# Kernel optimization log

Hardware: AMD Instinct MI355X
Metric: run time of the kernel (lower is better)

Reference implementation:

```python
import jax, jax.numpy as jnp
import numpy as np

EMBED_DIM = 256
H = 80
W = 80
N_HEADS = 8
N_POINTS = 4
B = 8


def sine_pe(C, h, w):
    # LoFTR-style PositionEncodingSine, returns [1, C, h, w]
    y_pos = jnp.cumsum(jnp.ones((h, w), jnp.float32), axis=0)[None]
    x_pos = jnp.cumsum(jnp.ones((h, w), jnp.float32), axis=1)[None]
    div = jnp.exp(jnp.arange(0, C // 2, 2, dtype=jnp.float32) * (-np.log(10000.0) / (C // 2)))[:, None, None]
    pe = jnp.zeros((C, h, w), jnp.float32)
    pe = pe.at[0::4].set(jnp.sin(x_pos * div))
    pe = pe.at[1::4].set(jnp.cos(x_pos * div))
    pe = pe.at[2::4].set(jnp.sin(y_pos * div))
    pe = pe.at[3::4].set(jnp.cos(y_pos * div))
    return pe[None]


def make_reference_points(h, w):
    # Faithful to the original (W-major flatten, (col, row) stacking)
    gr = np.linspace(0, 1, w)
    gc = np.linspace(0, 1, h)
    R, Cg = np.meshgrid(gr, gc, indexing='ij')  # (w, h)
    ref = np.stack((Cg, R), -1).reshape(-1, 2)  # [w*h, 2]
    return jnp.asarray(ref, jnp.float32)


def setup_inputs():
    key = jax.random.key(0)
    ks = jax.random.split(key, 8)
    C = EMBED_DIM
    s = 1.0 / np.sqrt(C)
    return {
        'query': jax.random.normal(ks[0], (B, C, H, W), jnp.float32),
        'value': jax.random.normal(ks[1], (B, C, H, W), jnp.float32),
        'W_value': jax.random.normal(ks[2], (C, C), jnp.float32) * s,
        'b_value': jnp.zeros((C,), jnp.float32),
        'W_off': jax.random.normal(ks[3], (C, N_HEADS * N_POINTS * 2), jnp.float32) * 0.01,
        'b_off': jax.random.normal(ks[4], (N_HEADS * N_POINTS * 2,), jnp.float32) * 0.5,
        'W_attn': jax.random.normal(ks[5], (C, N_HEADS * N_POINTS), jnp.float32) * s,
        'b_attn': jnp.zeros((N_HEADS * N_POINTS,), jnp.float32),
        'W_out': jax.random.normal(ks[6], (C, C), jnp.float32) * s,
        'b_out': jnp.zeros((C,), jnp.float32),
    }


def _deform_attn_core(q, v, ref, W_off, b_off, W_attn, b_attn):
    # q: [B, Nq, C] queries; v: [B, H*W, C] projected values; ref: [Nq, 2]
    Bq, Nq, C = q.shape
    hd = C // N_HEADS
    off = (q @ W_off + b_off).reshape(Bq, Nq, N_HEADS, N_POINTS, 2)
    aw = jax.nn.softmax((q @ W_attn + b_attn).reshape(Bq, Nq, N_HEADS, N_POINTS), axis=-1)
    norm = jnp.array([W, H], jnp.float32)  # offset normalizer (W, H), num_levels=1
    loc = ref[None, :, None, None, :] + off / norm  # [B, Nq, Hn, P, 2], normalized (x, y)
    loc = loc.transpose(0, 2, 1, 3, 4)  # [B, Hn, Nq, P, 2]
    # grid_sample(align_corners=False, padding_mode='zeros'): pixel = loc*size - 0.5
    x = loc[..., 0] * W - 0.5
    y = loc[..., 1] * H - 0.5
    x0f = jnp.floor(x); y0f = jnp.floor(y)
    wx = x - x0f; wy = y - y0f
    x0 = x0f.astype(jnp.int32); y0 = y0f.astype(jnp.int32)
    vh = v.reshape(Bq, H * W, N_HEADS, hd).transpose(0, 2, 1, 3)  # [B, Hn, HW, hd]

    def gather(ix, iy):
        valid = (ix >= 0) & (ix < W) & (iy >= 0) & (iy < H)
        idx = jnp.clip(iy, 0, H - 1) * W + jnp.clip(ix, 0, W - 1)  # [B, Hn, Nq, P]
        g = jnp.take_along_axis(vh, idx.reshape(Bq, N_HEADS, -1, 1), axis=2)
        return g.reshape(Bq, N_HEADS, Nq, N_POINTS, hd) * valid[..., None].astype(v.dtype)

    samp = (gather(x0, y0) * ((1 - wx) * (1 - wy))[..., None]
            + gather(x0 + 1, y0) * (wx * (1 - wy))[..., None]
            + gather(x0, y0 + 1) * ((1 - wx) * wy)[..., None]
            + gather(x0 + 1, y0 + 1) * (wx * wy)[..., None])  # [B, Hn, Nq, P, hd]
    out = jnp.einsum('bhqpd,bhqp->bqhd', samp, aw.transpose(0, 2, 1, 3))
    return out.reshape(Bq, Nq, C)


def reference(query, value, W_value, b_value, W_off, b_off, W_attn, b_attn, W_out, b_out):
    pe = sine_pe(EMBED_DIM, H, W)
    q = query + pe
    qf = q.reshape(B, EMBED_DIM, H * W).transpose(0, 2, 1)      # [B, Nq, C]
    vf = value.reshape(B, EMBED_DIM, H * W).transpose(0, 2, 1)  # [B, Nv, C]
    vproj = vf @ W_value + b_value
    ref = make_reference_points(H, W)
    attn = _deform_attn_core(qf, vproj, ref, W_off, b_off, W_attn, b_attn)
    attn = attn @ W_out + b_out
    attn = attn + qf  # mmcv MSDeformAttn residual (dropout identity at eval)
    out_img = attn.transpose(0, 2, 1).reshape(B, EMBED_DIM, H, W)
    # nn.Upsample(size=(H, W), bilinear) on an (H, W) map is identity (need_downsample=False)
    return (out_img + value, out_img)
```

## Files before the change

kernel.cpp:

```cpp
#include <hip/hip_runtime.h>
#include <hip/hip_bf16.h>
#include <stdint.h>

#define HH 80
#define WW 80
#define NQ 6400
#define CD 256
#define BB 8
#define OUT_HALF 13107200
#define PE_NEG 0.0719557841560639f

typedef __attribute__((ext_vector_type(4))) float f32x4;
typedef __bf16 bf16_t;
typedef __attribute__((ext_vector_type(8))) __bf16 bf16x8;

using gp1_t = const __attribute__((address_space(1))) void*;
using lp3_t = __attribute__((address_space(3))) void*;

__device__ __forceinline__ void gload_lds16(const void* g, void* l) {
    __builtin_amdgcn_global_load_lds((gp1_t)g, (lp3_t)l, 16, 0, 0);
}

__global__ __launch_bounds__(256) void wprep_kernel(const float* __restrict__ Wv,
                                                    const float* __restrict__ Woff,
                                                    const float* __restrict__ Wattn,
                                                    const float* __restrict__ Wout,
                                                    bf16_t* __restrict__ WvT,
                                                    bf16_t* __restrict__ WoaT,
                                                    bf16_t* __restrict__ WoT) {
    int idx = blockIdx.x * 256 + threadIdx.x;
    if (idx < 65536) {
        int cp = idx >> 8, c = idx & 255;
        WvT[idx] = (bf16_t)Wv[c * 256 + cp];
        WoT[idx] = (bf16_t)Wout[c * 256 + cp];
    }
    if (idx < 96 * 256) {
        int j = idx >> 8, c = idx & 255;
        WoaT[idx] = (bf16_t)(j < 64 ? Woff[c * 64 + j] : Wattn[c * 32 + (j - 64)]);
    }
}

__global__ __launch_bounds__(256, 3) void gemm_vproj(const float* __restrict__ V,
                                                     const bf16_t* __restrict__ Y,
                                                     const float* __restrict__ bias,
                                                     bf16_t* __restrict__ D) {
    __shared__ __align__(16) bf16_t lx[128 * 72];
    __shared__ __align__(16) bf16_t ly[128 * 64];
    int b = blockIdx.x & 7;
    int nloc = (blockIdx.x >> 3) * 128;
    int m0 = b * NQ + nloc;
    int c0 = blockIdx.y * 128;
    const float* src = V + (size_t)b * CD * NQ + nloc;
    int tid = threadIdx.x, wv = tid >> 6, ln = tid & 63;
    f32x4 acc[4][4] = {};
    int wr = (wv >> 1) * 64, wc = (wv & 1) * 64;
    int nl = tid & 31;
    for (int kt = 0; kt < 4; ++kt) {
#pragma unroll
        for (int q8 = 0; q8 < 4; ++q8) {
            int q = wv * 4 + q8;
            int row = q * 8 + (ln >> 3);
            int jj = (ln & 7) ^ (row & 7);
            gload_lds16((const char*)Y + ((size_t)(c0 + row)) * 512 + (size_t)kt * 128 + jj * 16,
                        (char*)ly + q * 1024);
        }
#pragma unroll
        for (int i = 0; i < 4; ++i) {
            int kp = (tid >> 5) + i * 8;
            int k = kp * 2;
            const float* s0 = src + (size_t)(kt * 64 + k) * NQ;
#pragma unroll
            for (int l = 0; l < 4; ++l) {
                int n = nl + 32 * l;
                float v0 = s0[n];
                float v1 = s0[NQ + n];
                union { bf16_t h[2]; uint32_t u; } pk;
                pk.h[0] = (bf16_t)v0; pk.h[1] = (bf16_t)v1;
                *(uint32_t*)((char*)lx + n * 144 + k * 2) = pk.u;
            }
        }
        __syncthreads();
#pragma unroll
        for (int ks = 0; ks < 2; ++ks) {
            bf16x8 xa[4], yb[4];
#pragma unroll
            for (int i = 0; i < 4; i++) {
                int m = wr + i * 16 + (ln & 15);
                xa[i] = *(const bf16x8*)((const char*)lx + m * 144 + ks * 64 + (ln >> 4) * 16);
                int n = wc + i * 16 + (ln & 15);
                int cn = (ks * 4 + (ln >> 4)) ^ (n & 7);
                yb[i] = *(const bf16x8*)((const char*)ly + n * 128 + cn * 16);
            }
#pragma unroll
            for (int i = 0; i < 4; i++)
#pragma unroll
                for (int j = 0; j < 4; j++)
                    acc[i][j] = __builtin_amdgcn_mfma_f32_16x16x32_bf16(xa[i], yb[j], acc[i][j], 0, 0, 0);
        }
        __syncthreads();
    }
#pragma unroll
    for (int i = 0; i < 4; i++)
#pragma unroll
        for (int j = 0; j < 4; j++) {
            int col = c0 + wc + j * 16 + (ln & 15);
            float bv = bias[col];
#pragma unroll
            for (int rg = 0; rg < 4; rg++) {
                int row = m0 + wr + i * 16 + (ln >> 4) * 4 + rg;
                D[(size_t)row * 256 + col] = (bf16_t)(acc[i][j][rg] + bv);
            }
        }
}

__global__ __launch_bounds__(256, 3) void oa_sample_out(
        const float* __restrict__ Q,
        const bf16_t* __restrict__ Woa,
        const float* __restrict__ boff,
        const float* __restrict__ battn,
        const bf16_t* __restrict__ vp,
        const bf16_t* __restrict__ WoT,
        const float* __restrict__ bout,
        const float* __restrict__ value,
        float* __restrict__ out) {
    __shared__ __align__(16) char smem[54272];
    char* sampL = smem;
    bf16_t* lx = (bf16_t*)(smem + 32768);
    bf16_t* ly = (bf16_t*)(smem + 41984);
    bf16_t* oaT = (bf16_t*)(smem + 32768);
    bf16_t* wx = (bf16_t*)(smem + 32768);
    float* tile = (float*)(smem + 32768);

    int bid = blockIdx.x;
    int b = bid & 7;
    int nloc = (bid >> 3) * 64;
    int tid = threadIdx.x, wv = tid >> 6, ln = tid & 63;
    const float* src = Q + (size_t)b * CD * NQ + nloc;
    int nl = tid & 31;

    f32x4 accA[6] = {};
    for (int kt = 0; kt < 4; ++kt) {
#pragma unroll
        for (int q3 = 0; q3 < 3; ++q3) {
            int q = wv * 3 + q3;
            int row = q * 8 + (ln >> 3);
            int jj = (ln & 7) ^ (row & 7);
            gload_lds16((const char*)Woa + ((size_t)row) * 512 + (size_t)kt * 128 + jj * 16,
                        (char*)ly + q * 1024);
        }
#pragma unroll
        for (int i = 0; i < 4; ++i) {
            int kp = (tid >> 5) + i * 8;
            int k = kp * 2;
            int c = kt * 64 + k;
            float d = __expf((float)(2 * (c >> 2)) * -PE_NEG);
            const float* s0 = src + (size_t)c * NQ;
#pragma unroll
            for (int l = 0; l < 2; ++l) {
                int n = nl + 32 * l;
                int p = nloc + n;
                int h = p / WW, w = p - h * WW;
                float pos = (c & 2) ? (float)(h + 1) : (float)(w + 1);
                float sv, cv;
                __sincosf(pos * d, &sv, &cv);
                float v0 = s0[n] + sv;
                float v1 = s0[NQ + n] + cv;
                union { bf16_t hh[2]; uint32_t u; } pk;
                pk.hh[0] = (bf16_t)v0; pk.hh[1] = (bf16_t)v1;
                *(uint32_t*)((char*)lx + n * 144 + k * 2) = pk.u;
            }
        }
        __syncthreads();
#pragma unroll
        for (int ks = 0; ks < 2; ++ks) {
            bf16x8 xa, yb[6];
            int m = wv * 16 + (ln & 15);
            xa = *(const bf16x8*)((const char*)lx + m * 144 + ks * 64 + (ln >> 4) * 16);
#pragma unroll
            for (int j = 0; j < 6; j++) {
                int n = j * 16 + (ln & 15);
                int cn = (ks * 4 + (ln >> 4)) ^ (n & 7);
                yb[j] = *(const bf16x8*)((const char*)ly + n * 128 + cn * 16);
            }
#pragma unroll
            for (int j = 0; j < 6; j++)
                accA[j] = __builtin_amdgcn_mfma_f32_16x16x32_bf16(xa, yb[j], accA[j], 0, 0, 0);
        }
        __syncthreads();
    }
#pragma unroll
    for (int j = 0; j < 6; j++) {
        int col = j * 16 + (ln & 15);
        float bv = col < 64 ? boff[col] : battn[col - 64];
#pragma unroll
        for (int rg = 0; rg < 4; rg++) {
            int rloc = wv * 16 + (ln >> 4) * 4 + rg;
            oaT[rloc * 100 + col] = (bf16_t)(accA[j][rg] + bv);
        }
    }
    __syncthreads();

    {
        int h = (tid >> 1) & 7, sh = tid & 1;
        const bf16_t* vb = vp + (size_t)b * NQ * CD + h * 32 + sh * 16;
#pragma unroll
        for (int rnd = 0; rnd < 4; ++rnd) {
            int q = rnd * 16 + (tid >> 4);
            int n = nloc + q;
            const bf16_t* sq = oaT + q * 100;
            float l0 = (float)sq[64 + h * 4 + 0], l1 = (float)sq[64 + h * 4 + 1];
            float l2 = (float)sq[64 + h * 4 + 2], l3 = (float)sq[64 + h * 4 + 3];
            float mx = fmaxf(fmaxf(l0, l1), fmaxf(l2, l3));
            float e0 = __expf(l0 - mx), e1 = __expf(l1 - mx), e2 = __expf(l2 - mx), e3 = __expf(l3 - mx);
            float inv = 1.f / (e0 + e1 + e2 + e3);
            float aw[4] = {e0 * inv, e1 * inv, e2 * inv, e3 * inv};
            float xb = (float)(n % WW) * (80.f / 79.f) - 0.5f;
            float yb = (float)(n / WW) * (80.f / 79.f) - 0.5f;
            float wgt[16];
            int idx[16];
#pragma unroll
            for (int p = 0; p < 4; p++) {
                float x = xb + (float)sq[h * 8 + p * 2];
                float y = yb + (float)sq[h * 8 + p * 2 + 1];
                float x0f = floorf(x), y0f = floorf(y);
                float wx_ = x - x0f, wy_ = y - y0f;
                int ix = (int)x0f, iy = (int)y0f;
                bool vx0 = (unsigned)ix < (unsigned)WW, vx1 = (unsigned)(ix + 1) < (unsigned)WW;
                bool vy0 = (unsigned)iy < (unsigned)HH, vy1 = (unsigned)(iy + 1) < (unsigned)HH;
                int cx0 = min(max(ix, 0), WW - 1), cx1 = min(max(ix + 1, 0), WW - 1);
                int cy0 = min(max(iy, 0), HH - 1), cy1 = min(max(iy + 1, 0), HH - 1);
                float ap = aw[p];
                wgt[p * 4 + 0] = (vx0 && vy0) ? ap * (1.f - wx_) * (1.f - wy_) : 0.f;
                wgt[p * 4 + 1] = (vx1 && vy0) ? ap * wx_ * (1.f - wy_) : 0.f;
                wgt[p * 4 + 2] = (vx0 && vy1) ? ap * (1.f - wx_) * wy_ : 0.f;
                wgt[p * 4 + 3] = (vx1 && vy1) ? ap * wx_ * wy_ : 0.f;
                idx[p * 4 + 0] = cy0 * WW + cx0;
                idx[p * 4 + 1] = cy0 * WW + cx1;
                idx[p * 4 + 2] = cy1 * WW + cx0;
                idx[p * 4 + 3] = cy1 * WW + cx1;
            }
            float fac[16];
#pragma unroll
            for (int j = 0; j < 16; j++) fac[j] = 0.f;
#pragma unroll
            for (int pc = 0; pc < 16; ++pc) {
                const bf16x8* p8 = (const bf16x8*)(vb + (size_t)idx[pc] * CD);
                bf16x8 v0 = p8[0], v1 = p8[1];
                float w = wgt[pc];
#pragma unroll
                for (int j = 0; j < 8; j++) fac[j] += (float)v0[j] * w;
#pragma unroll
                for (int j = 0; j < 8; j++) fac[8 + j] += (float)v1[j] * w;
            }
            bf16x8 o0, o1;
#pragma unroll
            for (int j = 0; j < 8; j++) { o0[j] = (bf16_t)fac[j]; o1[j] = (bf16_t)fac[8 + j]; }
            int c0 = 4 * h + 2 * sh;
            *(bf16x8*)(sampL + q * 512 + ((c0 ^ (q & 7)) * 16)) = o0;
            *(bf16x8*)(sampL + q * 512 + (((c0 + 1) ^ (q & 7)) * 16)) = o1;
        }
    }
    __syncthreads();

    const float* qp = Q + (size_t)b * CD * NQ;
    const float* vvp = value + (size_t)b * CD * NQ;
    float* o0p = out + (size_t)b * CD * NQ;
    float* o1p = out + OUT_HALF + (size_t)b * CD * NQ;
    for (int p = 0; p < 2; ++p) {
        int cb = p * 128;
        f32x4 acc[4][2] = {};
        for (int kt = 0; kt < 4; ++kt) {
#pragma unroll
            for (int q8 = 0; q8 < 4; ++q8) {
                int q = wv * 4 + q8;
                int row = q * 8 + (ln >> 3);
                int jj = (ln & 7) ^ (row & 7);
                gload_lds16((const char*)WoT + ((size_t)(cb + row)) * 512 + (size_t)kt * 128 + jj * 16,
                            (char*)wx + q * 1024);
            }
            __syncthreads();
#pragma unroll
            for (int ks = 0; ks < 2; ++ks) {
                bf16x8 xa[4], yb[2];
#pragma unroll
                for (int i = 0; i < 4; i++) {
                    int m = (wv >> 1) * 64 + i * 16 + (ln & 15);
                    int ch = (ks * 4 + (ln >> 4)) ^ (m & 7);
                    xa[i] = *(const bf16x8*)((const char*)wx + m * 128 + ch * 16);
                }
#pragma unroll
                for (int j = 0; j < 2; j++) {
                    int nr = (wv & 1) * 32 + j * 16 + (ln & 15);
                    int cj = kt * 8 + ks * 4 + (ln >> 4);
                    yb[j] = *(const bf16x8*)(sampL + nr * 512 + ((cj ^ (nr & 7)) * 16));
                }
#pragma unroll
                for (int i = 0; i < 4; i++)
#pragma unroll
                    for (int j = 0; j < 2; j++)
                        acc[i][j] = __builtin_amdgcn_mfma_f32_16x16x32_bf16(xa[i], yb[j], acc[i][j], 0, 0, 0);
            }
            __syncthreads();
        }
#pragma unroll
        for (int hp = 0; hp < 2; ++hp) {
            if ((wv >> 1) == hp) {
#pragma unroll
                for (int i = 0; i < 4; i++)
#pragma unroll
                    for (int j = 0; j < 2; j++) {
                        int c = (wv & 1) * 32 + j * 16 + (ln & 15);
#pragma unroll
                        for (int rg = 0; rg < 4; rg++) {
                            int r = i * 16 + (ln >> 4) * 4 + rg;
                            tile[r * 68 + c] = acc[i][j][rg] + bout[cb + hp * 64 + r];
                        }
                    }
            }
            __syncthreads();
            int g4 = (tid & 15) * 4;
            int rowbase = tid >> 4;
#pragma unroll
            for (int jj = 0; jj < 4; ++jj) {
                int r = rowbase + jj * 16;
                int crow = cb + hp * 64 + r;
                size_t off = (size_t)crow * NQ + nloc + g4;
                f32x4 tv = *(const f32x4*)&tile[r * 68 + g4];
                f32x4 qv = *(const f32x4*)(qp + off);
                f32x4 vv = *(const f32x4*)(vvp + off);
                float d = __expf((float)(2 * (crow >> 2)) * -PE_NEG);
                bool useY = (crow & 2) != 0, odd = (crow & 1) != 0;
                f32x4 pv;
#pragma unroll
                for (int e = 0; e < 4; ++e) {
                    int n = nloc + g4 + e;
                    int hh = n / WW, ww = n - hh * WW;
                    float pos = useY ? (float)(hh + 1) : (float)(ww + 1);
                    float sv, cv;
                    __sincosf(pos * d, &sv, &cv);
                    pv[e] = odd ? cv : sv;
                }
                f32x4 o1v = tv + qv + pv;
                *(f32x4*)(o1p + off) = o1v;
                *(f32x4*)(o0p + off) = o1v + vv;
            }
            __syncthreads();
        }
    }
}

extern "C" void kernel_launch(void* const* d_in, const int* in_sizes, int n_in,
                              void* d_out, int out_size, void* d_ws, size_t ws_size,
                              hipStream_t stream) {
    const float* query   = (const float*)d_in[0];
    const float* value   = (const float*)d_in[1];
    const float* W_value = (const float*)d_in[2];
    const float* b_value = (const float*)d_in[3];
    const float* W_off   = (const float*)d_in[4];
    const float* b_off   = (const float*)d_in[5];
    const float* W_attn  = (const float*)d_in[6];
    const float* b_attn  = (const float*)d_in[7];
    const float* W_out   = (const float*)d_in[8];
    const float* b_out   = (const float*)d_in[9];
    float* out = (float*)d_out;
    char* ws = (char*)d_ws;

    bf16_t* WvT   = (bf16_t*)(ws + 0);
    bf16_t* WoT   = (bf16_t*)(ws + 131072);
    bf16_t* WoaT  = (bf16_t*)(ws + 262144);
    bf16_t* vprojB= (bf16_t*)(ws + 311296);

    wprep_kernel<<<256, 256, 0, stream>>>(W_value, W_off, W_attn, W_out, WvT, WoaT, WoT);
    gemm_vproj<<<dim3(400, 2), 256, 0, stream>>>(value, WvT, b_value, vprojB);
    oa_sample_out<<<800, 256, 0, stream>>>(query, WoaT, b_off, b_attn, vprojB,
                                           WoT, b_out, value, out);
}
```

Before: 104.2 us.

## Prefetch full-K W_out slice during sampling and restructure output GEMM into 64-row passes

The output projection now loads a whole 64x256 slice of the transposed W_out into LDS at once instead of streaming it in K-tiles. The first slice is issued asynchronously before the bilinear sampling phase so the load overlaps the gathers. oaT moves to its own LDS region so the prefetch does not overwrite it. The GEMM runs as four 64-channel passes with one wave per 16 rows, which removes the per-K-tile barriers. The cost is a larger LDS footprint (about 78KB), so occupancy bounds drop from 3 to 2 blocks per CU, and each later slice load sits between passes without overlap.

```diff
diff --git a/kernel.cpp b/kernel.cpp
--- a/kernel.cpp
+++ b/kernel.cpp
@@ -113,7 +113,7 @@
         }
 }
 
-__global__ __launch_bounds__(256, 3) void oa_sample_out(
+__global__ __launch_bounds__(256, 2) void oa_sample_out(
         const float* __restrict__ Q,
         const bf16_t* __restrict__ Woa,
         const float* __restrict__ boff,
@@ -123,13 +123,13 @@
         const float* __restrict__ bout,
         const float* __restrict__ value,
         float* __restrict__ out) {
-    __shared__ __align__(16) char smem[54272];
+    __shared__ __align__(16) char smem[78336];
     char* sampL = smem;
     bf16_t* lx = (bf16_t*)(smem + 32768);
     bf16_t* ly = (bf16_t*)(smem + 41984);
-    bf16_t* oaT = (bf16_t*)(smem + 32768);
-    bf16_t* wx = (bf16_t*)(smem + 32768);
+    char* wx = smem + 32768;
     float* tile = (float*)(smem + 32768);
+    bf16_t* oaT = (bf16_t*)(smem + 65536);
 
     int bid = blockIdx.x;
     int b = bid & 7;
@@ -199,6 +199,14 @@
         }
     }
     __syncthreads();
+
+#pragma unroll
+    for (int i = 0; i < 8; ++i) {
+        int rr = (wv * 8 + i) * 2 + (ln >> 5);
+        int jj = (ln & 31) ^ (rr & 7);
+        gload_lds16((const char*)WoT + ((size_t)rr) * 512 + jj * 16,
+                    wx + (wv * 8 + i) * 1024);
+    }
 
     {
         int h = (tid >> 1) & 7, sh = tid & 1;
@@ -266,83 +274,68 @@
     const float* vvp = value + (size_t)b * CD * NQ;
     float* o0p = out + (size_t)b * CD * NQ;
     float* o1p = out + OUT_HALF + (size_t)b * CD * NQ;
-    for (int p = 0; p < 2; ++p) {
-        int cb = p * 128;
-        f32x4 acc[4][2] = {};
-        for (int kt = 0; kt < 4; ++kt) {
-#pragma unroll
-            for (int q8 = 0; q8 < 4; ++q8) {
-                int q = wv * 4 + q8;
-                int row = q * 8 + (ln >> 3);
-                int jj = (ln & 7) ^ (row & 7);
-                gload_lds16((const char*)WoT + ((size_t)(cb + row)) * 512 + (size_t)kt * 128 + jj * 16,
-                            (char*)wx + q * 1024);
-            }
-            __syncthreads();
-#pragma unroll
-            for (int ks = 0; ks < 2; ++ks) {
-                bf16x8 xa[4], yb[2];
-#pragma unroll
-                for (int i = 0; i < 4; i++) {
-                    int m = (wv >> 1) * 64 + i * 16 + (ln & 15);
-                    int ch = (ks * 4 + (ln >> 4)) ^ (m & 7);
-                    xa[i] = *(const bf16x8*)((const char*)wx + m * 128 + ch * 16);
-                }
-#pragma unroll
-                for (int j = 0; j < 2; j++) {
-                    int nr = (wv & 1) * 32 + j * 16 + (ln & 15);
-                    int cj = kt * 8 + ks * 4 + (ln >> 4);
-                    yb[j] = *(const bf16x8*)(sampL + nr * 512 + ((cj ^ (nr & 7)) * 16));
-                }
-#pragma unroll
-                for (int i = 0; i < 4; i++)
-#pragma unroll
-                    for (int j = 0; j < 2; j++)
-                        acc[i][j] = __builtin_amdgcn_mfma_f32_16x16x32_bf16(xa[i], yb[j], acc[i][j], 0, 0, 0);
-            }
-            __syncthreads();
-        }
-#pragma unroll
-        for (int hp = 0; hp < 2; ++hp) {
-            if ((wv >> 1) == hp) {
-#pragma unroll
-                for (int i = 0; i < 4; i++)
-#pragma unroll
-                    for (int j = 0; j < 2; j++) {
-                        int c = (wv & 1) * 32 + j * 16 + (ln & 15);
-#pragma unroll
-                        for (int rg = 0; rg < 4; rg++) {
-                            int r = i * 16 + (ln >> 4) * 4 + rg;
-                            tile[r * 68 + c] = acc[i][j][rg] + bout[cb + hp * 64 + r];
-                        }
-                    }
-            }
-            __syncthreads();
-            int g4 = (tid & 15) * 4;
-            int rowbase = tid >> 4;
-#pragma unroll
-            for (int jj = 0; jj < 4; ++jj) {
-                int r = rowbase + jj * 16;
-                int crow = cb + hp * 64 + r;
-                size_t off = (size_t)crow * NQ + nloc + g4;
-                f32x4 tv = *(const f32x4*)&tile[r * 68 + g4];
-                f32x4 qv = *(const f32x4*)(qp + off);
-                f32x4 vv = *(const f32x4*)(vvp + off);
-                float d = __expf((float)(2 * (crow >> 2)) * -PE_NEG);
-                bool useY = (crow & 2) != 0, odd = (crow & 1) != 0;
-                f32x4 pv;
-#pragma unroll
-                for (int e = 0; e < 4; ++e) {
-                    int n = nloc + g4 + e;
-                    int hh = n / WW, ww = n - hh * WW;
-                    float pos = useY ? (float)(hh + 1) : (float)(ww + 1);
-                    float sv, cv;
-                    __sincosf(pos * d, &sv, &cv);
-                    pv[e] = odd ? cv : sv;
-                }
-                f32x4 o1v = tv + qv + pv;
-                *(f32x4*)(o1p + off) = o1v;
-                *(f32x4*)(o0p + off) = o1v + vv;
+    for (int p = 0; p < 4; ++p) {
+        f32x4 acc[4] = {};
+        int m = wv * 16 + (ln & 15);
+#pragma unroll
+        for (int ks2 = 0; ks2 < 8; ++ks2) {
+            bf16x8 xa, yb[4];
+            int kc = ks2 * 4 + (ln >> 4);
+            xa = *(const bf16x8*)(wx + m * 512 + ((kc ^ (m & 7)) * 16));
+#pragma unroll
+            for (int j = 0; j < 4; j++) {
+                int nr = j * 16 + (ln & 15);
+                yb[j] = *(const bf16x8*)(sampL + nr * 512 + ((kc ^ (nr & 7)) * 16));
+            }
+#pragma unroll
+            for (int j = 0; j < 4; j++)
+                acc[j] = __builtin_amdgcn_mfma_f32_16x16x32_bf16(xa, yb[j], acc[j], 0, 0, 0);
+        }
+        __syncthreads();
+#pragma unroll
+        for (int j = 0; j < 4; j++) {
+            int c = j * 16 + (ln & 15);
+#pragma unroll
+            for (int rg = 0; rg < 4; rg++) {
+                int r = wv * 16 + (ln >> 4) * 4 + rg;
+                tile[r * 68 + c] = acc[j][rg] + bout[p * 64 + r];
+            }
+        }
+        __syncthreads();
+        int g4 = (tid & 15) * 4;
+        int rowbase = tid >> 4;
+#pragma unroll
+        for (int jj2 = 0; jj2 < 4; ++jj2) {
+            int r = rowbase + jj2 * 16;
+            int crow = p * 64 + r;
+            size_t off = (size_t)crow * NQ + nloc + g4;
+            f32x4 tv = *(const f32x4*)&tile[r * 68 + g4];
+            f32x4 qv = *(const f32x4*)(qp + off);
+            f32x4 vv = *(const f32x4*)(vvp + off);
+            float d = __expf((float)(2 * (crow >> 2)) * -PE_NEG);
+            bool useY = (crow & 2) != 0, odd = (crow & 1) != 0;
+            f32x4 pv;
+#pragma unroll
+            for (int e = 0; e < 4; ++e) {
+                int n = nloc + g4 + e;
+                int hh = n / WW, ww = n - hh * WW;
+                float pos = useY ? (float)(hh + 1) : (float)(ww + 1);
+                float sv, cv;
+                __sincosf(pos * d, &sv, &cv);
+                pv[e] = odd ? cv : sv;
+            }
+            f32x4 o1v = tv + qv + pv;
+            *(f32x4*)(o1p + off) = o1v;
+            *(f32x4*)(o0p + off) = o1v + vv;
+        }
+        __syncthreads();
+        if (p < 3) {
+#pragma unroll
+            for (int i = 0; i < 8; ++i) {
+                int rr = (wv * 8 + i) * 2 + (ln >> 5);
+                int jj = (ln & 31) ^ (rr & 7);
+                gload_lds16((const char*)WoT + ((size_t)((p + 1) * 64 + rr)) * 512 + jj * 16,
+                            wx + (wv * 8 + i) * 1024);
             }
             __syncthreads();
         }
```

New measurement: 101.8 us (median of 2 runs). 1.02x faster.
